# Performance work log

Measured on AMD Instinct MI355X. Metric: run time of the kernel, lower is better.

Reference implementation:

```python
import jax, jax.numpy as jnp
import numpy as np


def _gcn_conv(x, src, dst, num_nodes, W, b):
    # GCNConv (PyG defaults): h = D^{-1/2} (A + I) D^{-1/2} (x @ W) + b
    h = x @ W  # [N, F_out]
    ones = jnp.ones(src.shape[0], dtype=h.dtype)
    deg = jax.ops.segment_sum(ones, dst, num_segments=num_nodes)  # in-degree incl. self loop
    dinv = jnp.where(deg > 0, jax.lax.rsqrt(deg), 0.0)
    norm = dinv[src] * dinv[dst]  # [E+N]
    msg = h[src] * norm[:, None]  # gather + scale (memory-bound)
    out = jax.ops.segment_sum(msg, dst, num_segments=num_nodes)
    return out + b


def setup_inputs() -> dict:
    key = jax.random.key(0)
    k1, k2, k3, k4 = jax.random.split(key, 4)
    N, E, D_IN, D_H, D_OUT = 100000, 1600000, 128, 64, 32
    x = jax.random.normal(k1, (N, D_IN), dtype=jnp.float32)
    edge_index = jax.random.randint(k2, (2, E), 0, N, dtype=jnp.int64)
    # Glorot-style init for weights, zero bias (as PyG reset_parameters)
    W1 = jax.random.normal(k3, (D_IN, D_H), dtype=jnp.float32) * (2.0 / (D_IN + D_H)) ** 0.5
    b1 = jnp.zeros((D_H,), dtype=jnp.float32)
    W2 = jax.random.normal(k4, (D_H, D_OUT), dtype=jnp.float32) * (2.0 / (D_H + D_OUT)) ** 0.5
    b2 = jnp.zeros((D_OUT,), dtype=jnp.float32)
    return {"x": x, "edge_index": edge_index, "W1": W1, "b1": b1, "W2": W2, "b2": b2}


def reference(x, edge_index, W1, b1, W2, b2):
    num_nodes = x.shape[0]
    # add self loops once (GCNConv default add_self_loops=True)
    loop = jnp.arange(num_nodes, dtype=edge_index.dtype)
    src = jnp.concatenate([edge_index[0], loop])
    dst = jnp.concatenate([edge_index[1], loop])
    h = jax.nn.relu(_gcn_conv(x, src, dst, num_nodes, W1, b1))
    # F.dropout(training=self.training): eval mode -> identity
    out = _gcn_conv(h, src, dst, num_nodes, W2, b2)
    return out
```

## Files before the change

kernel.cpp:

```cpp
#include <hip/hip_runtime.h>
#include <math.h>


#define THREADS 256
#define HTHREADS 512
#define PBLK 256
#define BSHIFT 8
#define AGG_NODES 64
#define CSR_LDS 2048

typedef _Float16 h8v __attribute__((ext_vector_type(8)));
typedef _Float16 h4v __attribute__((ext_vector_type(4)));
typedef float f32x4 __attribute__((ext_vector_type(4)));

__device__ __forceinline__ int nt_ld_i(const int* p) {
    return __builtin_nontemporal_load(p);
}

__device__ __forceinline__ int detect64_block(const int* __restrict__ idx, int E,
                                              int* s_flag) {
    if (threadIdx.x == 0) *s_flag = 1;
    __syncthreads();
    int n = (E < 1024) ? E : 1024;
    for (int i = threadIdx.x; i < n; i += blockDim.x)
        if (idx[2 * i + 1] != 0) *s_flag = 0;
    __syncthreads();
    return *s_flag;
}

__global__ __launch_bounds__(HTHREADS) void k_hist(const int* __restrict__ idx, int E,
                                                   int* __restrict__ bh, int NB) {
    extern __shared__ int lh[];
    int is64 = detect64_block(idx, E, &lh[NB]);
    for (int t = threadIdx.x; t < NB; t += HTHREADS) lh[t] = 0;
    __syncthreads();
    int chunk = (E + PBLK - 1) / PBLK;
    int start = blockIdx.x * chunk;
    int end = min(start + chunk, E);
    for (int e = start + threadIdx.x; e < end; e += HTHREADS) {
        int d = is64 ? idx[2 * E + 2 * e] : idx[E + e];
        atomicAdd(&lh[d >> BSHIFT], 1);
    }
    __syncthreads();
    for (int t = threadIdx.x; t < NB; t += HTHREADS)
        bh[blockIdx.x * NB + t] = lh[t];
}

__global__ __launch_bounds__(THREADS) void k_colsum(const int* __restrict__ bh,
                                                    int* __restrict__ bcnt, int NB) {
    __shared__ int ws[4];
    int b = blockIdx.x;
    int v = bh[threadIdx.x * NB + b];
    int lane = threadIdx.x & 63, w = threadIdx.x >> 6;
#pragma unroll
    for (int o = 32; o; o >>= 1) v += __shfl_down(v, o);
    if (lane == 0) ws[w] = v;
    __syncthreads();
    if (threadIdx.x == 0) bcnt[b] = ws[0] + ws[1] + ws[2] + ws[3];
}

__global__ __launch_bounds__(THREADS) void k_scan(const int* __restrict__ cnt,
                                                  int* __restrict__ off, int NB) {
    __shared__ int wsum[4];
    __shared__ int carry_s;
    if (threadIdx.x == 0) carry_s = 0;
    __syncthreads();
    int t = threadIdx.x, lane = t & 63, w = t >> 6;
    for (int base = 0; base < NB; base += THREADS) {
        int i = base + t;
        int raw = (i < NB) ? cnt[i] : 0;
        int v = raw;
#pragma unroll
        for (int o = 1; o < 64; o <<= 1) {
            int u = __shfl_up(v, o);
            if (lane >= o) v += u;
        }
        if (lane == 63) wsum[w] = v;
        __syncthreads();
        int c0 = carry_s;
        int wadd = 0;
#pragma unroll
        for (int k = 0; k < 4; ++k) if (k < w) wadd += wsum[k];
        if (i < NB) off[i] = v - raw + wadd + c0;
        __syncthreads();
        if (t == 0) carry_s += wsum[0] + wsum[1] + wsum[2] + wsum[3];
        __syncthreads();
    }
    if (t == 0) off[NB] = carry_s;
}

__global__ __launch_bounds__(64) void k_bbase(const int* __restrict__ bh,
                                              const int* __restrict__ boff,
                                              int* __restrict__ bbase, int NB) {
    int b = blockIdx.x;
    int lane = threadIdx.x;
    int carry = boff[b];
    for (int base = 0; base < PBLK; base += 64) {
        int idx = (base + lane) * NB + b;
        int raw = bh[idx];
        int v = raw;
#pragma unroll
        for (int o = 1; o < 64; o <<= 1) {
            int u = __shfl_up(v, o);
            if (lane >= o) v += u;
        }
        bbase[idx] = carry + v - raw;
        carry += __shfl(v, 63);
    }
}

__global__ __launch_bounds__(HTHREADS) void k_partition(const int* __restrict__ idx, int E,
                                                        const int* __restrict__ bbase,
                                                        unsigned* __restrict__ pairs, int NB) {
    extern __shared__ int sm[];
    int* lbase = sm;
    int* lcur  = sm + NB;
    int is64 = detect64_block(idx, E, &lcur[NB]);
    for (int t = threadIdx.x; t < NB; t += HTHREADS) {
        lbase[t] = bbase[blockIdx.x * NB + t];
        lcur[t] = 0;
    }
    __syncthreads();
    int chunk = (E + PBLK - 1) / PBLK;
    int start = blockIdx.x * chunk;
    int end = min(start + chunk, E);
    for (int e = start + threadIdx.x; e < end; e += HTHREADS) {
        int s = is64 ? idx[2 * e] : idx[e];
        int d = is64 ? idx[2 * E + 2 * e] : idx[E + e];
        int b = d >> BSHIFT;
        int r = atomicAdd(&lcur[b], 1);
        pairs[lbase[b] + r] = (unsigned)s | ((unsigned)(d & 255) << 24);
    }
}

__global__ __launch_bounds__(THREADS) void k_sort(const unsigned* __restrict__ pairs,
                                                  const int* __restrict__ boff,
                                                  int* __restrict__ csr_src,
                                                  int* __restrict__ row_ptr,
                                                  float* __restrict__ dinv, int N, int NB) {
    __shared__ int cnt[256];
    __shared__ int cur[256];
    __shared__ int wsum[4];
    const int b = blockIdx.x, t = threadIdx.x;
    const int start = boff[b], end = boff[b + 1];
    cnt[t] = 0;
    __syncthreads();
    for (int j = start + t; j < end; j += THREADS)
        atomicAdd(&cnt[pairs[j] >> 24], 1);
    __syncthreads();
    int deg = cnt[t];
    int lane = t & 63, w = t >> 6;
    int v = deg;
#pragma unroll
    for (int o = 1; o < 64; o <<= 1) {
        int u = __shfl_up(v, o);
        if (lane >= o) v += u;
    }
    if (lane == 63) wsum[w] = v;
    __syncthreads();
    int wadd = 0;
#pragma unroll
    for (int k = 0; k < 4; ++k) if (k < w) wadd += wsum[k];
    int pos = start + (v - deg) + wadd;
    cur[t] = pos;
    int node = (b << BSHIFT) + t;
    if (node < N) {
        row_ptr[node] = pos;
        dinv[node] = rsqrtf((float)(deg + 1));
    }
    if (b == NB - 1 && t == 0) row_ptr[N] = end;
    __syncthreads();
    for (int j = start + t; j < end; j += THREADS) {
        unsigned p = pairs[j];
        int r = atomicAdd(&cur[p >> 24], 1);
        csr_src[r] = (int)(p & 0xFFFFFFu);
    }
}

__global__ __launch_bounds__(THREADS) void k_gemm1(const float* __restrict__ x,
                                                   const float* __restrict__ W,
                                                   const float* __restrict__ dinv,
                                                   _Float16* __restrict__ h, int N) {
    __shared__ _Float16 xs[64][136];
    __shared__ _Float16 wsT[64][136];
    const int tid = threadIdx.x;
    const int brow = blockIdx.x * 64;
    for (int f = tid; f < 64 * 32; f += THREADS) {
        int r = f >> 5, c4 = (f & 31) << 2;
        int row = brow + r;
        float4 v = make_float4(0.f, 0.f, 0.f, 0.f);
        if (row < N) v = *(const float4*)&x[(size_t)row * 128 + c4];
        h4v hv;
        hv.x = (_Float16)v.x; hv.y = (_Float16)v.y;
        hv.z = (_Float16)v.z; hv.w = (_Float16)v.w;
        *(h4v*)&xs[r][c4] = hv;
    }
    for (int f = tid; f < 128 * 16; f += THREADS) {
        int k = f >> 4, n4 = (f & 15) << 2;
        float4 w = *(const float4*)&W[(size_t)k * 64 + n4];
        wsT[n4 + 0][k] = (_Float16)w.x;
        wsT[n4 + 1][k] = (_Float16)w.y;
        wsT[n4 + 2][k] = (_Float16)w.z;
        wsT[n4 + 3][k] = (_Float16)w.w;
    }
    __syncthreads();
    const int wv = tid >> 6, lane = tid & 63;
    const int fr = lane & 15;
    const int kg = lane >> 4;
    f32x4 acc[4];
    acc[0] = acc[1] = acc[2] = acc[3] = (f32x4){0.f, 0.f, 0.f, 0.f};
#pragma unroll
    for (int ks = 0; ks < 4; ++ks) {
        h8v a = *(const h8v*)&xs[(wv << 4) + fr][(kg << 3) + (ks << 5)];
#pragma unroll
        for (int c = 0; c < 4; ++c) {
            h8v b = *(const h8v*)&wsT[(c << 4) + fr][(kg << 3) + (ks << 5)];
            acc[c] = __builtin_amdgcn_mfma_f32_16x16x32_f16(a, b, acc[c], 0, 0, 0);
        }
    }
#pragma unroll
    for (int i = 0; i < 4; ++i) {
        int row = brow + (wv << 4) + (kg << 2) + i;
        if (row < N) {
            float dn = dinv[row];
#pragma unroll
            for (int c = 0; c < 4; ++c)
                h[(size_t)row * 64 + (c << 4) + fr] = (_Float16)(acc[c][i] * dn);
        }
    }
}

__global__ __launch_bounds__(THREADS) void k_agg1f(const int* __restrict__ row_ptr,
                                                   const int* __restrict__ csr,
                                                   const float* __restrict__ dinv,
                                                   const _Float16* __restrict__ hs,
                                                   const float* __restrict__ b1,
                                                   const float* __restrict__ W2,
                                                   _Float16* __restrict__ h2s, int N) {
    __shared__ float w2s[64][32];
    __shared__ float rowbuf[4][8][68];
    __shared__ int rp_s[AGG_NODES + 1];
    __shared__ float dinv_s[AGG_NODES];
    __shared__ int csr_s[CSR_LDS];
    const int tid = threadIdx.x;
    for (int f = tid; f < 64 * 8; f += THREADS) {
        int k = f >> 3, c4 = (f & 7) << 2;
        *(float4*)&w2s[k][c4] = *(const float4*)&W2[(size_t)k * 32 + c4];
    }
    const int nbase = blockIdx.x * AGG_NODES;
    const int nend = min(nbase + AGG_NODES, N);
    const int ncnt = nend - nbase;
    if (tid <= ncnt) rp_s[tid] = row_ptr[nbase + tid];
    if (tid < ncnt) dinv_s[tid] = dinv[nbase + tid];
    __syncthreads();
    const int seg0 = rp_s[0];
    const int seglen = rp_s[ncnt] - seg0;
    const bool inlds = (seglen <= CSR_LDS);
    if (inlds)
        for (int t = tid; t < seglen; t += THREADS) csr_s[t] = nt_ld_i(&csr[seg0 + t]);
    __syncthreads();

    const int wv = tid >> 6, lane = tid & 63;
    const int g = lane >> 3, fl = lane & 7;
    const int fb = fl << 3;

    for (int c = 0; c < 2; ++c) {
        const int nloc = (wv << 4) + (c << 3) + g;
        const bool act = (nloc < ncnt);
        const int node = nbase + nloc;
        const int start = act ? rp_s[nloc] : 0;
        const int end = act ? rp_s[nloc + 1] : 0;
        h8v acc0 = {0, 0, 0, 0, 0, 0, 0, 0};
        h8v acc1 = {0, 0, 0, 0, 0, 0, 0, 0};
        if (act) acc0 = *(const h8v*)&hs[(size_t)node * 64 + fb];
        if (inlds) {
            int j = start - seg0;
            const int e_ = end - seg0;
            for (; j + 1 < e_; j += 2) {
                int s0 = csr_s[j], s1 = csr_s[j + 1];
                acc0 += *(const h8v*)&hs[(size_t)s0 * 64 + fb];
                acc1 += *(const h8v*)&hs[(size_t)s1 * 64 + fb];
            }
            if (j < e_) acc0 += *(const h8v*)&hs[(size_t)csr_s[j] * 64 + fb];
        } else {
            int j = start;
            for (; j + 1 < end; j += 2) {
                int s0 = nt_ld_i(&csr[j]), s1 = nt_ld_i(&csr[j + 1]);
                acc0 += *(const h8v*)&hs[(size_t)s0 * 64 + fb];
                acc1 += *(const h8v*)&hs[(size_t)s1 * 64 + fb];
            }
            if (j < end) acc0 += *(const h8v*)&hs[(size_t)nt_ld_i(&csr[j]) * 64 + fb];
        }
        if (act) {
            const float dn = dinv_s[nloc];
            float4 bb0 = *(const float4*)&b1[fb];
            float4 bb1 = *(const float4*)&b1[fb + 4];
            float4 r0, r1;
            r0.x = fmaxf(dn * ((float)acc0[0] + (float)acc1[0]) + bb0.x, 0.f);
            r0.y = fmaxf(dn * ((float)acc0[1] + (float)acc1[1]) + bb0.y, 0.f);
            r0.z = fmaxf(dn * ((float)acc0[2] + (float)acc1[2]) + bb0.z, 0.f);
            r0.w = fmaxf(dn * ((float)acc0[3] + (float)acc1[3]) + bb0.w, 0.f);
            r1.x = fmaxf(dn * ((float)acc0[4] + (float)acc1[4]) + bb1.x, 0.f);
            r1.y = fmaxf(dn * ((float)acc0[5] + (float)acc1[5]) + bb1.y, 0.f);
            r1.z = fmaxf(dn * ((float)acc0[6] + (float)acc1[6]) + bb1.z, 0.f);
            r1.w = fmaxf(dn * ((float)acc0[7] + (float)acc1[7]) + bb1.w, 0.f);
            *(float4*)&rowbuf[wv][g][fb] = r0;
            *(float4*)&rowbuf[wv][g][fb + 4] = r1;
        }
        if (act) {
            float a0 = 0.f, a1 = 0.f, a2 = 0.f, a3 = 0.f;
            const int cb = fl << 2;
#pragma unroll
            for (int k = 0; k < 64; ++k) {
                float r = rowbuf[wv][g][k];
                a0 += r * w2s[k][cb + 0];
                a1 += r * w2s[k][cb + 1];
                a2 += r * w2s[k][cb + 2];
                a3 += r * w2s[k][cb + 3];
            }
            const float dn = dinv_s[nloc];
            h4v hv;
            hv.x = (_Float16)(dn * a0);
            hv.y = (_Float16)(dn * a1);
            hv.z = (_Float16)(dn * a2);
            hv.w = (_Float16)(dn * a3);
            *(h4v*)&h2s[(size_t)node * 32 + cb] = hv;
        }
    }
}

__global__ __launch_bounds__(THREADS) void k_agg2(const int* __restrict__ row_ptr,
                                                  const int* __restrict__ csr,
                                                  const float* __restrict__ dinv,
                                                  const _Float16* __restrict__ hs,
                                                  const float* __restrict__ b2,
                                                  float* __restrict__ out, int N) {
    __shared__ int rp_s[AGG_NODES + 1];
    __shared__ float dinv_s[AGG_NODES];
    __shared__ int csr_s[CSR_LDS];
    const int tid = threadIdx.x;
    const int nbase = blockIdx.x * AGG_NODES;
    const int nend = min(nbase + AGG_NODES, N);
    const int ncnt = nend - nbase;
    if (tid <= ncnt) rp_s[tid] = row_ptr[nbase + tid];
    if (tid < ncnt) dinv_s[tid] = dinv[nbase + tid];
    __syncthreads();
    const int seg0 = rp_s[0];
    const int seglen = rp_s[ncnt] - seg0;
    const bool inlds = (seglen <= CSR_LDS);
    if (inlds)
        for (int t = tid; t < seglen; t += THREADS) csr_s[t] = nt_ld_i(&csr[seg0 + t]);
    __syncthreads();

    const int wv = tid >> 6, lane = tid & 63;
    const int g = lane >> 2, fl = lane & 3;
    const int fb = fl << 3;

    const int nloc = (wv << 4) + g;
    const bool act = (nloc < ncnt);
    const int node = nbase + nloc;
    const int start = act ? rp_s[nloc] : 0;
    const int end = act ? rp_s[nloc + 1] : 0;
    h8v acc0 = {0, 0, 0, 0, 0, 0, 0, 0};
    h8v acc1 = {0, 0, 0, 0, 0, 0, 0, 0};
    if (act) acc0 = *(const h8v*)&hs[(size_t)node * 32 + fb];
    if (inlds) {
        int j = start - seg0;
        const int e_ = end - seg0;
        for (; j + 1 < e_; j += 2) {
            int s0 = csr_s[j], s1 = csr_s[j + 1];
            acc0 += *(const h8v*)&hs[(size_t)s0 * 32 + fb];
            acc1 += *(const h8v*)&hs[(size_t)s1 * 32 + fb];
        }
        if (j < e_) acc0 += *(const h8v*)&hs[(size_t)csr_s[j] * 32 + fb];
    } else {
        int j = start;
        for (; j + 1 < end; j += 2) {
            int s0 = nt_ld_i(&csr[j]), s1 = nt_ld_i(&csr[j + 1]);
            acc0 += *(const h8v*)&hs[(size_t)s0 * 32 + fb];
            acc1 += *(const h8v*)&hs[(size_t)s1 * 32 + fb];
        }
        if (j < end) acc0 += *(const h8v*)&hs[(size_t)nt_ld_i(&csr[j]) * 32 + fb];
    }
    if (act) {
        const float dn = dinv_s[nloc];
        float4 bb0 = *(const float4*)&b2[fb];
        float4 bb1 = *(const float4*)&b2[fb + 4];
        float4 r0, r1;
        r0.x = dn * ((float)acc0[0] + (float)acc1[0]) + bb0.x;
        r0.y = dn * ((float)acc0[1] + (float)acc1[1]) + bb0.y;
        r0.z = dn * ((float)acc0[2] + (float)acc1[2]) + bb0.z;
        r0.w = dn * ((float)acc0[3] + (float)acc1[3]) + bb0.w;
        r1.x = dn * ((float)acc0[4] + (float)acc1[4]) + bb1.x;
        r1.y = dn * ((float)acc0[5] + (float)acc1[5]) + bb1.y;
        r1.z = dn * ((float)acc0[6] + (float)acc1[6]) + bb1.z;
        r1.w = dn * ((float)acc0[7] + (float)acc1[7]) + bb1.w;
        *(float4*)&out[(size_t)node * 32 + fb] = r0;
        *(float4*)&out[(size_t)node * 32 + fb + 4] = r1;
    }
}

extern "C" void kernel_launch(void* const* d_in, const int* in_sizes, int n_in,
                              void* d_out, int out_size, void* d_ws, size_t ws_size,
                              hipStream_t stream) {
    const int N = in_sizes[0] / 128;
    const int E = in_sizes[1] / 2;
    const float* x  = (const float*)d_in[0];
    const int*   ei = (const int*)d_in[1];
    const float* W1 = (const float*)d_in[2];
    const float* b1 = (const float*)d_in[3];
    const float* W2 = (const float*)d_in[4];
    const float* b2 = (const float*)d_in[5];
    float* out = (float*)d_out;

    const int NB = (N + 255) >> BSHIFT;

    float*     dinv    = (float*)d_ws;
    _Float16*  h1b     = (_Float16*)(dinv + N);
    _Float16*  h2b     = h1b + (size_t)N * 64;
    int*       csr_src = (int*)(h2b + (size_t)N * 32);
    int*       row_ptr = csr_src + E;
    int*       bh      = row_ptr + N + 1;
    int*       bbase   = bh + (size_t)PBLK * NB;
    int*       bcnt    = bbase + (size_t)PBLK * NB;
    int*       boff    = bcnt + NB;
    unsigned*  pairs   = (unsigned*)h1b;

    k_hist<<<PBLK, HTHREADS, (NB + 1) * 4, stream>>>(ei, E, bh, NB);
    k_colsum<<<NB, THREADS, 0, stream>>>(bh, bcnt, NB);
    k_scan<<<1, THREADS, 0, stream>>>(bcnt, boff, NB);
    k_bbase<<<NB, 64, 0, stream>>>(bh, boff, bbase, NB);
    k_partition<<<PBLK, HTHREADS, (2 * NB + 1) * 4, stream>>>(ei, E, bbase, pairs, NB);
    k_sort<<<NB, THREADS, 0, stream>>>(pairs, boff, csr_src, row_ptr, dinv, N, NB);

    k_gemm1<<<(N + 63) / 64, THREADS, 0, stream>>>(x, W1, dinv, h1b, N);
    const int ablk = (N + AGG_NODES - 1) / AGG_NODES;
    k_agg1f<<<ablk, THREADS, 0, stream>>>(row_ptr, csr_src, dinv, h1b, b1, W2, h2b, N);
    k_agg2<<<ablk, THREADS, 0, stream>>>(row_ptr, csr_src, dinv, h2b, b2, out, N);
}
```

Measured before the change: 128.1 us.

## Slab feature layout for aggregation, split agg1 fusion into separate MFMA gemm2

Stores the hidden features in feature-slab-major layout (8 halves per node per slab), so each aggregation block gathers one 16-byte slab per neighbor and its random gathers hit a smaller working set. Each aggregation block handles 128 nodes with 512 threads, and four lanes per node split the edges, combined with xor shuffles. The previously fused aggregate-then-W2 step becomes a separate aggregation kernel plus an MFMA gemm2 kernel. This adds an extra kernel, extra workspace, and repeats the CSR/row_ptr loads across slab blocks. PBLK is doubled, and colsum is updated to sum two histogram rows per thread.

```diff
diff --git a/kernel.cpp b/kernel.cpp
--- a/kernel.cpp
+++ b/kernel.cpp
@@ -4,10 +4,11 @@
 
 #define THREADS 256
 #define HTHREADS 512
-#define PBLK 256
+#define ATHREADS 512
+#define PBLK 512
 #define BSHIFT 8
-#define AGG_NODES 64
-#define CSR_LDS 2048
+#define AGG_NODES 128
+#define CSR_LDS 3072
 
 typedef _Float16 h8v __attribute__((ext_vector_type(8)));
 typedef _Float16 h4v __attribute__((ext_vector_type(4)));
@@ -15,6 +16,14 @@
 
 __device__ __forceinline__ int nt_ld_i(const int* p) {
     return __builtin_nontemporal_load(p);
+}
+
+__device__ __forceinline__ h8v shfl_xor_h8(h8v v, int off) {
+    union { h8v h; int i[4]; } u, r;
+    u.h = v;
+#pragma unroll
+    for (int k = 0; k < 4; ++k) r.i[k] = __shfl_xor(u.i[k], off);
+    return r.h;
 }
 
 __device__ __forceinline__ int detect64_block(const int* __restrict__ idx, int E,
@@ -50,7 +59,7 @@
                                                     int* __restrict__ bcnt, int NB) {
     __shared__ int ws[4];
     int b = blockIdx.x;
-    int v = bh[threadIdx.x * NB + b];
+    int v = bh[threadIdx.x * NB + b] + bh[(threadIdx.x + THREADS) * NB + b];
     int lane = threadIdx.x & 63, w = threadIdx.x >> 6;
 #pragma unroll
     for (int o = 32; o; o >>= 1) v += __shfl_down(v, o);
@@ -224,30 +233,27 @@
         if (row < N) {
             float dn = dinv[row];
 #pragma unroll
-            for (int c = 0; c < 4; ++c)
-                h[(size_t)row * 64 + (c << 4) + fr] = (_Float16)(acc[c][i] * dn);
-        }
-    }
-}
-
-__global__ __launch_bounds__(THREADS) void k_agg1f(const int* __restrict__ row_ptr,
-                                                   const int* __restrict__ csr,
-                                                   const float* __restrict__ dinv,
-                                                   const _Float16* __restrict__ hs,
-                                                   const float* __restrict__ b1,
-                                                   const float* __restrict__ W2,
-                                                   _Float16* __restrict__ h2s, int N) {
-    __shared__ float w2s[64][32];
-    __shared__ float rowbuf[4][8][68];
+            for (int c = 0; c < 4; ++c) {
+                int col = (c << 4) + fr;
+                h[((size_t)(col >> 3) * N + row) * 8 + (col & 7)] =
+                    (_Float16)(acc[c][i] * dn);
+            }
+        }
+    }
+}
+
+__global__ __launch_bounds__(ATHREADS) void k_agg1s(const int* __restrict__ row_ptr,
+                                                    const int* __restrict__ csr,
+                                                    const float* __restrict__ dinv,
+                                                    const _Float16* __restrict__ hs,
+                                                    const float* __restrict__ b1,
+                                                    _Float16* __restrict__ o1, int N) {
     __shared__ int rp_s[AGG_NODES + 1];
     __shared__ float dinv_s[AGG_NODES];
     __shared__ int csr_s[CSR_LDS];
     const int tid = threadIdx.x;
-    for (int f = tid; f < 64 * 8; f += THREADS) {
-        int k = f >> 3, c4 = (f & 7) << 2;
-        *(float4*)&w2s[k][c4] = *(const float4*)&W2[(size_t)k * 32 + c4];
-    }
-    const int nbase = blockIdx.x * AGG_NODES;
+    const int s = blockIdx.x & 7;
+    const int nbase = (blockIdx.x >> 3) * AGG_NODES;
     const int nend = min(nbase + AGG_NODES, N);
     const int ncnt = nend - nbase;
     if (tid <= ncnt) rp_s[tid] = row_ptr[nbase + tid];
@@ -257,144 +263,185 @@
     const int seglen = rp_s[ncnt] - seg0;
     const bool inlds = (seglen <= CSR_LDS);
     if (inlds)
-        for (int t = tid; t < seglen; t += THREADS) csr_s[t] = nt_ld_i(&csr[seg0 + t]);
-    __syncthreads();
-
-    const int wv = tid >> 6, lane = tid & 63;
-    const int g = lane >> 3, fl = lane & 7;
-    const int fb = fl << 3;
-
-    for (int c = 0; c < 2; ++c) {
-        const int nloc = (wv << 4) + (c << 3) + g;
-        const bool act = (nloc < ncnt);
-        const int node = nbase + nloc;
-        const int start = act ? rp_s[nloc] : 0;
-        const int end = act ? rp_s[nloc + 1] : 0;
-        h8v acc0 = {0, 0, 0, 0, 0, 0, 0, 0};
-        h8v acc1 = {0, 0, 0, 0, 0, 0, 0, 0};
-        if (act) acc0 = *(const h8v*)&hs[(size_t)node * 64 + fb];
-        if (inlds) {
-            int j = start - seg0;
-            const int e_ = end - seg0;
-            for (; j + 1 < e_; j += 2) {
-                int s0 = csr_s[j], s1 = csr_s[j + 1];
-                acc0 += *(const h8v*)&hs[(size_t)s0 * 64 + fb];
-                acc1 += *(const h8v*)&hs[(size_t)s1 * 64 + fb];
-            }
-            if (j < e_) acc0 += *(const h8v*)&hs[(size_t)csr_s[j] * 64 + fb];
-        } else {
-            int j = start;
-            for (; j + 1 < end; j += 2) {
-                int s0 = nt_ld_i(&csr[j]), s1 = nt_ld_i(&csr[j + 1]);
-                acc0 += *(const h8v*)&hs[(size_t)s0 * 64 + fb];
-                acc1 += *(const h8v*)&hs[(size_t)s1 * 64 + fb];
-            }
-            if (j < end) acc0 += *(const h8v*)&hs[(size_t)nt_ld_i(&csr[j]) * 64 + fb];
-        }
-        if (act) {
-            const float dn = dinv_s[nloc];
-            float4 bb0 = *(const float4*)&b1[fb];
-            float4 bb1 = *(const float4*)&b1[fb + 4];
-            float4 r0, r1;
-            r0.x = fmaxf(dn * ((float)acc0[0] + (float)acc1[0]) + bb0.x, 0.f);
-            r0.y = fmaxf(dn * ((float)acc0[1] + (float)acc1[1]) + bb0.y, 0.f);
-            r0.z = fmaxf(dn * ((float)acc0[2] + (float)acc1[2]) + bb0.z, 0.f);
-            r0.w = fmaxf(dn * ((float)acc0[3] + (float)acc1[3]) + bb0.w, 0.f);
-            r1.x = fmaxf(dn * ((float)acc0[4] + (float)acc1[4]) + bb1.x, 0.f);
-            r1.y = fmaxf(dn * ((float)acc0[5] + (float)acc1[5]) + bb1.y, 0.f);
-            r1.z = fmaxf(dn * ((float)acc0[6] + (float)acc1[6]) + bb1.z, 0.f);
-            r1.w = fmaxf(dn * ((float)acc0[7] + (float)acc1[7]) + bb1.w, 0.f);
-            *(float4*)&rowbuf[wv][g][fb] = r0;
-            *(float4*)&rowbuf[wv][g][fb + 4] = r1;
-        }
-        if (act) {
-            float a0 = 0.f, a1 = 0.f, a2 = 0.f, a3 = 0.f;
-            const int cb = fl << 2;
-#pragma unroll
-            for (int k = 0; k < 64; ++k) {
-                float r = rowbuf[wv][g][k];
-                a0 += r * w2s[k][cb + 0];
-                a1 += r * w2s[k][cb + 1];
-                a2 += r * w2s[k][cb + 2];
-                a3 += r * w2s[k][cb + 3];
-            }
-            const float dn = dinv_s[nloc];
-            h4v hv;
-            hv.x = (_Float16)(dn * a0);
-            hv.y = (_Float16)(dn * a1);
-            hv.z = (_Float16)(dn * a2);
-            hv.w = (_Float16)(dn * a3);
-            *(h4v*)&h2s[(size_t)node * 32 + cb] = hv;
-        }
-    }
-}
-
-__global__ __launch_bounds__(THREADS) void k_agg2(const int* __restrict__ row_ptr,
-                                                  const int* __restrict__ csr,
-                                                  const float* __restrict__ dinv,
-                                                  const _Float16* __restrict__ hs,
-                                                  const float* __restrict__ b2,
-                                                  float* __restrict__ out, int N) {
-    __shared__ int rp_s[AGG_NODES + 1];
-    __shared__ float dinv_s[AGG_NODES];
-    __shared__ int csr_s[CSR_LDS];
-    const int tid = threadIdx.x;
-    const int nbase = blockIdx.x * AGG_NODES;
-    const int nend = min(nbase + AGG_NODES, N);
-    const int ncnt = nend - nbase;
-    if (tid <= ncnt) rp_s[tid] = row_ptr[nbase + tid];
-    if (tid < ncnt) dinv_s[tid] = dinv[nbase + tid];
-    __syncthreads();
-    const int seg0 = rp_s[0];
-    const int seglen = rp_s[ncnt] - seg0;
-    const bool inlds = (seglen <= CSR_LDS);
-    if (inlds)
-        for (int t = tid; t < seglen; t += THREADS) csr_s[t] = nt_ld_i(&csr[seg0 + t]);
-    __syncthreads();
-
+        for (int t = tid; t < seglen; t += ATHREADS) csr_s[t] = nt_ld_i(&csr[seg0 + t]);
+    __syncthreads();
+
+    const _Float16* hslab = hs + (size_t)s * N * 8;
     const int wv = tid >> 6, lane = tid & 63;
     const int g = lane >> 2, fl = lane & 3;
-    const int fb = fl << 3;
 
     const int nloc = (wv << 4) + g;
     const bool act = (nloc < ncnt);
     const int node = nbase + nloc;
     const int start = act ? rp_s[nloc] : 0;
     const int end = act ? rp_s[nloc + 1] : 0;
-    h8v acc0 = {0, 0, 0, 0, 0, 0, 0, 0};
-    h8v acc1 = {0, 0, 0, 0, 0, 0, 0, 0};
-    if (act) acc0 = *(const h8v*)&hs[(size_t)node * 32 + fb];
+    h8v a0 = {0, 0, 0, 0, 0, 0, 0, 0};
+    h8v a1 = a0;
+    if (act && fl == 0) a0 = *(const h8v*)&hslab[(size_t)node * 8];
     if (inlds) {
-        int j = start - seg0;
+        int j = start - seg0 + fl;
         const int e_ = end - seg0;
-        for (; j + 1 < e_; j += 2) {
-            int s0 = csr_s[j], s1 = csr_s[j + 1];
-            acc0 += *(const h8v*)&hs[(size_t)s0 * 32 + fb];
-            acc1 += *(const h8v*)&hs[(size_t)s1 * 32 + fb];
-        }
-        if (j < e_) acc0 += *(const h8v*)&hs[(size_t)csr_s[j] * 32 + fb];
+        for (; j + 4 < e_; j += 8) {
+            int s0 = csr_s[j], s1 = csr_s[j + 4];
+            a0 += *(const h8v*)&hslab[(size_t)s0 * 8];
+            a1 += *(const h8v*)&hslab[(size_t)s1 * 8];
+        }
+        if (j < e_) a0 += *(const h8v*)&hslab[(size_t)csr_s[j] * 8];
     } else {
-        int j = start;
-        for (; j + 1 < end; j += 2) {
-            int s0 = nt_ld_i(&csr[j]), s1 = nt_ld_i(&csr[j + 1]);
-            acc0 += *(const h8v*)&hs[(size_t)s0 * 32 + fb];
-            acc1 += *(const h8v*)&hs[(size_t)s1 * 32 + fb];
-        }
-        if (j < end) acc0 += *(const h8v*)&hs[(size_t)nt_ld_i(&csr[j]) * 32 + fb];
-    }
-    if (act) {
+        int j = start + fl;
+        for (; j + 4 < end; j += 8) {
+            int s0 = nt_ld_i(&csr[j]), s1 = nt_ld_i(&csr[j + 4]);
+            a0 += *(const h8v*)&hslab[(size_t)s0 * 8];
+            a1 += *(const h8v*)&hslab[(size_t)s1 * 8];
+        }
+        if (j < end) a0 += *(const h8v*)&hslab[(size_t)nt_ld_i(&csr[j]) * 8];
+    }
+    a0 += a1;
+    a0 += shfl_xor_h8(a0, 1);
+    a0 += shfl_xor_h8(a0, 2);
+    if (act && fl == 0) {
         const float dn = dinv_s[nloc];
+        const int fb = s << 3;
+        float4 bb0 = *(const float4*)&b1[fb];
+        float4 bb1 = *(const float4*)&b1[fb + 4];
+        h8v o;
+        o[0] = (_Float16)fmaxf(dn * (float)a0[0] + bb0.x, 0.f);
+        o[1] = (_Float16)fmaxf(dn * (float)a0[1] + bb0.y, 0.f);
+        o[2] = (_Float16)fmaxf(dn * (float)a0[2] + bb0.z, 0.f);
+        o[3] = (_Float16)fmaxf(dn * (float)a0[3] + bb0.w, 0.f);
+        o[4] = (_Float16)fmaxf(dn * (float)a0[4] + bb1.x, 0.f);
+        o[5] = (_Float16)fmaxf(dn * (float)a0[5] + bb1.y, 0.f);
+        o[6] = (_Float16)fmaxf(dn * (float)a0[6] + bb1.z, 0.f);
+        o[7] = (_Float16)fmaxf(dn * (float)a0[7] + bb1.w, 0.f);
+        *(h8v*)&o1[((size_t)s * N + node) * 8] = o;
+    }
+}
+
+__global__ __launch_bounds__(THREADS) void k_gemm2(const _Float16* __restrict__ o1,
+                                                   const float* __restrict__ W,
+                                                   const float* __restrict__ dinv,
+                                                   _Float16* __restrict__ h2, int N) {
+    __shared__ _Float16 xs[128][72];
+    __shared__ _Float16 wsT[32][72];
+    const int tid = threadIdx.x;
+    const int brow = blockIdx.x * 128;
+    for (int f = tid; f < 1024; f += THREADS) {
+        int s = f >> 7, row = f & 127;
+        h8v v = {0, 0, 0, 0, 0, 0, 0, 0};
+        if (brow + row < N) v = *(const h8v*)&o1[((size_t)s * N + brow + row) * 8];
+        *(h8v*)&xs[row][s << 3] = v;
+    }
+    for (int f = tid; f < 64 * 32; f += THREADS) {
+        int k = f >> 5, c = f & 31;
+        wsT[c][k] = (_Float16)W[(size_t)k * 32 + c];
+    }
+    __syncthreads();
+    const int wv = tid >> 6, lane = tid & 63;
+    const int fr = lane & 15;
+    const int kg = lane >> 4;
+    f32x4 acc[2][2];
+    acc[0][0] = acc[0][1] = acc[1][0] = acc[1][1] = (f32x4){0.f, 0.f, 0.f, 0.f};
+#pragma unroll
+    for (int rt = 0; rt < 2; ++rt) {
+#pragma unroll
+        for (int ks = 0; ks < 2; ++ks) {
+            h8v a = *(const h8v*)&xs[(wv << 5) + (rt << 4) + fr][(kg << 3) + (ks << 5)];
+#pragma unroll
+            for (int ct = 0; ct < 2; ++ct) {
+                h8v b = *(const h8v*)&wsT[(ct << 4) + fr][(kg << 3) + (ks << 5)];
+                acc[rt][ct] = __builtin_amdgcn_mfma_f32_16x16x32_f16(a, b, acc[rt][ct], 0, 0, 0);
+            }
+        }
+    }
+#pragma unroll
+    for (int rt = 0; rt < 2; ++rt) {
+#pragma unroll
+        for (int i = 0; i < 4; ++i) {
+            int row = brow + (wv << 5) + (rt << 4) + (kg << 2) + i;
+            if (row < N) {
+                float dn = dinv[row];
+#pragma unroll
+                for (int ct = 0; ct < 2; ++ct) {
+                    int col = (ct << 4) + fr;
+                    h2[((size_t)(col >> 3) * N + row) * 8 + (col & 7)] =
+                        (_Float16)(acc[rt][ct][i] * dn);
+                }
+            }
+        }
+    }
+}
+
+__global__ __launch_bounds__(ATHREADS) void k_agg2s(const int* __restrict__ row_ptr,
+                                                    const int* __restrict__ csr,
+                                                    const float* __restrict__ dinv,
+                                                    const _Float16* __restrict__ hs,
+                                                    const float* __restrict__ b2,
+                                                    float* __restrict__ out, int N) {
+    __shared__ int rp_s[AGG_NODES + 1];
+    __shared__ float dinv_s[AGG_NODES];
+    __shared__ int csr_s[CSR_LDS];
+    const int tid = threadIdx.x;
+    const int s = blockIdx.x & 3;
+    const int nbase = (blockIdx.x >> 2) * AGG_NODES;
+    const int nend = min(nbase + AGG_NODES, N);
+    const int ncnt = nend - nbase;
+    if (tid <= ncnt) rp_s[tid] = row_ptr[nbase + tid];
+    if (tid < ncnt) dinv_s[tid] = dinv[nbase + tid];
+    __syncthreads();
+    const int seg0 = rp_s[0];
+    const int seglen = rp_s[ncnt] - seg0;
+    const bool inlds = (seglen <= CSR_LDS);
+    if (inlds)
+        for (int t = tid; t < seglen; t += ATHREADS) csr_s[t] = nt_ld_i(&csr[seg0 + t]);
+    __syncthreads();
+
+    const _Float16* hslab = hs + (size_t)s * N * 8;
+    const int wv = tid >> 6, lane = tid & 63;
+    const int g = lane >> 2, fl = lane & 3;
+
+    const int nloc = (wv << 4) + g;
+    const bool act = (nloc < ncnt);
+    const int node = nbase + nloc;
+    const int start = act ? rp_s[nloc] : 0;
+    const int end = act ? rp_s[nloc + 1] : 0;
+    h8v a0 = {0, 0, 0, 0, 0, 0, 0, 0};
+    h8v a1 = a0;
+    if (act && fl == 0) a0 = *(const h8v*)&hslab[(size_t)node * 8];
+    if (inlds) {
+        int j = start - seg0 + fl;
+        const int e_ = end - seg0;
+        for (; j + 4 < e_; j += 8) {
+            int s0 = csr_s[j], s1 = csr_s[j + 4];
+            a0 += *(const h8v*)&hslab[(size_t)s0 * 8];
+            a1 += *(const h8v*)&hslab[(size_t)s1 * 8];
+        }
+        if (j < e_) a0 += *(const h8v*)&hslab[(size_t)csr_s[j] * 8];
+    } else {
+        int j = start + fl;
+        for (; j + 4 < end; j += 8) {
+            int s0 = nt_ld_i(&csr[j]), s1 = nt_ld_i(&csr[j + 4]);
+            a0 += *(const h8v*)&hslab[(size_t)s0 * 8];
+            a1 += *(const h8v*)&hslab[(size_t)s1 * 8];
+        }
+        if (j < end) a0 += *(const h8v*)&hslab[(size_t)nt_ld_i(&csr[j]) * 8];
+    }
+    a0 += a1;
+    a0 += shfl_xor_h8(a0, 1);
+    a0 += shfl_xor_h8(a0, 2);
+    if (act && fl == 0) {
+        const float dn = dinv_s[nloc];
+        const int fb = s << 3;
         float4 bb0 = *(const float4*)&b2[fb];
         float4 bb1 = *(const float4*)&b2[fb + 4];
         float4 r0, r1;
-        r0.x = dn * ((float)acc0[0] + (float)acc1[0]) + bb0.x;
-        r0.y = dn * ((float)acc0[1] + (float)acc1[1]) + bb0.y;
-        r0.z = dn * ((float)acc0[2] + (float)acc1[2]) + bb0.z;
-        r0.w = dn * ((float)acc0[3] + (float)acc1[3]) + bb0.w;
-        r1.x = dn * ((float)acc0[4] + (float)acc1[4]) + bb1.x;
-        r1.y = dn * ((float)acc0[5] + (float)acc1[5]) + bb1.y;
-        r1.z = dn * ((float)acc0[6] + (float)acc1[6]) + bb1.z;
-        r1.w = dn * ((float)acc0[7] + (float)acc1[7]) + bb1.w;
+        r0.x = dn * (float)a0[0] + bb0.x;
+        r0.y = dn * (float)a0[1] + bb0.y;
+        r0.z = dn * (float)a0[2] + bb0.z;
+        r0.w = dn * (float)a0[3] + bb0.w;
+        r1.x = dn * (float)a0[4] + bb1.x;
+        r1.y = dn * (float)a0[5] + bb1.y;
+        r1.z = dn * (float)a0[6] + bb1.z;
+        r1.w = dn * (float)a0[7] + bb1.w;
         *(float4*)&out[(size_t)node * 32 + fb] = r0;
         *(float4*)&out[(size_t)node * 32 + fb + 4] = r1;
     }
@@ -417,7 +464,8 @@
 
     float*     dinv    = (float*)d_ws;
     _Float16*  h1b     = (_Float16*)(dinv + N);
-    _Float16*  h2b     = h1b + (size_t)N * 64;
+    _Float16*  o1b     = h1b + (size_t)N * 64;
+    _Float16*  h2b     = o1b + (size_t)N * 64;
     int*       csr_src = (int*)(h2b + (size_t)N * 32);
     int*       row_ptr = csr_src + E;
     int*       bh      = row_ptr + N + 1;
@@ -434,7 +482,8 @@
     k_sort<<<NB, THREADS, 0, stream>>>(pairs, boff, csr_src, row_ptr, dinv, N, NB);
 
     k_gemm1<<<(N + 63) / 64, THREADS, 0, stream>>>(x, W1, dinv, h1b, N);
-    const int ablk = (N + AGG_NODES - 1) / AGG_NODES;
-    k_agg1f<<<ablk, THREADS, 0, stream>>>(row_ptr, csr_src, dinv, h1b, b1, W2, h2b, N);
-    k_agg2<<<ablk, THREADS, 0, stream>>>(row_ptr, csr_src, dinv, h2b, b2, out, N);
-}
+    const int nb128 = (N + AGG_NODES - 1) / AGG_NODES;
+    k_agg1s<<<nb128 * 8, ATHREADS, 0, stream>>>(row_ptr, csr_src, dinv, h1b, b1, o1b, N);
+    k_gemm2<<<nb128, THREADS, 0, stream>>>(o1b, W2, dinv, h2b, N);
+    k_agg2s<<<nb128 * 4, ATHREADS, 0, stream>>>(row_ptr, csr_src, dinv, h2b, b2, out, N);
+}
```

New measurement: 198.3 us. 54.8% more time.
